# Optimization experiments

Measured on AMD Instinct MI355X. Metric: run time of the kernel, lower is better.

Reference implementation:

```python
import jax, jax.numpy as jnp
import numpy as np

NEG_SLOPE = 0.01  # nn.LeakyReLU default


def leaky_relu(x):
    return jnp.where(x >= 0, x, NEG_SLOPE * x)


def gcn_conv(x, W, b, src, dst, n_nodes):
    """PyG GCNConv: add self loops, symmetric D^-1/2 (A+I) D^-1/2 norm, then x @ W + b."""
    h = x @ W  # [N, D]
    # degree with self-loops (edge weight 1 each, +1 for the self loop)
    deg = jnp.zeros((n_nodes,), dtype=x.dtype).at[dst].add(1.0) + 1.0
    dinv = jax.lax.rsqrt(deg)  # deg >= 1 thanks to self loops
    norm = dinv[src] * dinv[dst]  # [E]
    msg = h[src] * norm[:, None]  # gather + scale, [E, D]
    agg = jnp.zeros_like(h).at[dst].add(msg)  # scatter-add over targets
    agg = agg + h * (dinv * dinv)[:, None]  # self-loop contribution
    return agg + b


def setup_inputs() -> dict:
    key = jax.random.key(0)
    ks = jax.random.split(key, 12)
    N, E = 100000, 640000
    ND, D, C = 239, 128, 2
    x = jax.random.normal(ks[0], (N, ND), dtype=jnp.float32)
    edge_index = jax.random.randint(ks[1], (2, E), 0, N, dtype=jnp.int64)
    edge_type = jax.random.randint(ks[2], (E,), 0, 4, dtype=jnp.int64)
    s = 0.05
    W_in = jax.random.normal(ks[3], (ND, D), dtype=jnp.float32) * s
    b_in = jax.random.normal(ks[4], (D,), dtype=jnp.float32) * s
    W_g = jax.random.normal(ks[5], (D, D), dtype=jnp.float32) * s
    b_g = jax.random.normal(ks[6], (D,), dtype=jnp.float32) * s
    W_o1 = jax.random.normal(ks[7], (D, D), dtype=jnp.float32) * s
    b_o1 = jax.random.normal(ks[8], (D,), dtype=jnp.float32) * s
    W_o2 = jax.random.normal(ks[9], (D, C), dtype=jnp.float32) * s
    b_o2 = jax.random.normal(ks[10], (C,), dtype=jnp.float32) * s
    return {"x": x, "edge_index": edge_index, "edge_type": edge_type,
            "W_in": W_in, "b_in": b_in, "W_g": W_g, "b_g": b_g,
            "W_o1": W_o1, "b_o1": b_o1, "W_o2": W_o2, "b_o2": b_o2}


def reference(x, edge_index, edge_type, W_in, b_in, W_g, b_g, W_o1, b_o1, W_o2, b_o2):
    n_nodes = x.shape[0]
    src, dst = edge_index[0], edge_index[1]
    h = leaky_relu(x @ W_in + b_in)
    h = gcn_conv(h, W_g, b_g, src, dst, n_nodes)
    # dropout is identity in eval mode (training=False)
    h = gcn_conv(h, W_g, b_g, src, dst, n_nodes)  # same shared GCNConv instance
    h = leaky_relu(h @ W_o1 + b_o1)
    return h @ W_o2 + b_o2
```

## Files before the change

kernel.cpp:

```cpp
#include <hip/hip_runtime.h>
#include <hip/hip_bf16.h>


typedef __attribute__((ext_vector_type(8))) __bf16 bf16x8;
typedef __attribute__((ext_vector_type(4))) float f32x4;

__global__ __launch_bounds__(256) void wtr_k(const float* __restrict__ W, ushort* __restrict__ Wt,
                                             int K, int Kp) {
  int idx = blockIdx.x * 256 + threadIdx.x;
  if (idx >= 128 * Kp) return;
  int n = idx / Kp, k = idx % Kp;
  float v = (k < K) ? W[(size_t)k * 128 + n] : 0.f;
  __hip_bfloat16 h = __float2bfloat16(v);
  Wt[idx] = *(ushort*)&h;
}


__global__ __launch_bounds__(256) void zero_k(int* __restrict__ p, int n) {
  int i = blockIdx.x * 256 + threadIdx.x;
  if (i < n) p[i] = 0;
}

__global__ __launch_bounds__(256) void hist_k(const int* __restrict__ dst, int* __restrict__ cnt, int E) {
  int e = blockIdx.x * 256 + threadIdx.x;
  if (e < E) atomicAdd(&cnt[dst[e]], 1);
}

__global__ __launch_bounds__(256) void scan1_k(const int* __restrict__ cnt, int* __restrict__ rp,
                                               int* __restrict__ bsum, int N) {
  __shared__ int sd[256];
  int t = threadIdx.x;
  int base = blockIdx.x * 1024 + t * 4;
  int v0 = (base + 0 < N) ? cnt[base + 0] : 0;
  int v1 = (base + 1 < N) ? cnt[base + 1] : 0;
  int v2 = (base + 2 < N) ? cnt[base + 2] : 0;
  int v3 = (base + 3 < N) ? cnt[base + 3] : 0;
  int ts = v0 + v1 + v2 + v3;
  sd[t] = ts;
  __syncthreads();
  for (int off = 1; off < 256; off <<= 1) {
    int y = (t >= off) ? sd[t - off] : 0;
    __syncthreads();
    sd[t] += y;
    __syncthreads();
  }
  int x = sd[t] - ts;
  if (t == 255) bsum[blockIdx.x] = sd[255];
  if (base + 0 < N) rp[base + 0] = x; x += v0;
  if (base + 1 < N) rp[base + 1] = x; x += v1;
  if (base + 2 < N) rp[base + 2] = x; x += v2;
  if (base + 3 < N) rp[base + 3] = x;
}

__global__ __launch_bounds__(256) void scan2_k(int* __restrict__ bsum, int NB) {
  __shared__ int sd[256];
  int t = threadIdx.x;
  int base = t * 4;
  int v0 = (base + 0 < NB) ? bsum[base + 0] : 0;
  int v1 = (base + 1 < NB) ? bsum[base + 1] : 0;
  int v2 = (base + 2 < NB) ? bsum[base + 2] : 0;
  int v3 = (base + 3 < NB) ? bsum[base + 3] : 0;
  int ts = v0 + v1 + v2 + v3;
  sd[t] = ts;
  __syncthreads();
  for (int off = 1; off < 256; off <<= 1) {
    int y = (t >= off) ? sd[t - off] : 0;
    __syncthreads();
    sd[t] += y;
    __syncthreads();
  }
  int x = sd[t] - ts;
  if (base + 0 < NB) bsum[base + 0] = x; x += v0;
  if (base + 1 < NB) bsum[base + 1] = x; x += v1;
  if (base + 2 < NB) bsum[base + 2] = x; x += v2;
  if (base + 3 < NB) bsum[base + 3] = x;
}

__global__ __launch_bounds__(256) void scan3_k(int* __restrict__ rp, int* __restrict__ pos,
                                               const int* __restrict__ bsum,
                                               float* __restrict__ dinv, int N, int E) {
  int i = blockIdx.x * 256 + threadIdx.x;
  if (i < N) {
    int c = pos[i];
    int v = rp[i] + bsum[i >> 10];
    dinv[i] = rsqrtf((float)c + 1.0f);
    rp[i] = v;
    pos[i] = v;
  }
  if (i == 0) rp[N] = E;
}

__global__ __launch_bounds__(256) void fill_k(const int* __restrict__ src, const int* __restrict__ dst,
                                              const float* __restrict__ dinv,
                                              int* __restrict__ pos, int2* __restrict__ ew, int E) {
  int e = blockIdx.x * 256 + threadIdx.x;
  if (e < E) {
    int d = dst[e];
    int s = src[e];
    int idx = atomicAdd(&pos[d], 1);
    ew[idx] = make_int2(s, __float_as_int(dinv[s] * dinv[d]));
  }
}


__global__ __launch_bounds__(512, 4) void gemm1_k(const float* __restrict__ x,
                                                  const ushort* __restrict__ Wt,
                                                  const float* __restrict__ bias,
                                                  ushort* __restrict__ C, int N, int Ka,
                                                  unsigned long long M ) {
  __shared__ ushort Al[128 * 248];
  __shared__ ushort Wl[128 * 72];
  const int tid = threadIdx.x;
  const int wave = tid >> 6;
  const int lane = tid & 63;
  const int l16 = lane & 15;
  const int quad = lane >> 4;
  const int m0 = blockIdx.x * 128;

  if (tid < 128) {
    Al[tid * 248 + 239] = 0;
    *(uint4*)&Al[tid * 248 + 240] = make_uint4(0, 0, 0, 0);
  }

  {
    int rows = N - m0;
    if (rows > 128) rows = 128;
    const int region = rows * Ka;
    const float* __restrict__ xb = x + (size_t)m0 * Ka;
    const int nv4 = region >> 2;
    for (int i = tid; i < nv4; i += 512) {
      float4 v = ((const float4*)xb)[i];
      int f0 = i * 4;
      float vf[4] = {v.x, v.y, v.z, v.w};
#pragma unroll
      for (int j = 0; j < 4; ++j) {
        int idx = f0 + j;
        uint r = (uint)(((unsigned long long)(uint)idx * M) >> 40);
        uint c = (uint)idx - r * (uint)Ka;
        __hip_bfloat16 h = __float2bfloat16(vf[j]);
        Al[r * 248 + c] = *(ushort*)&h;
      }
    }
    for (int i = (nv4 << 2) + tid; i < region; i += 512) {
      uint r = (uint)(((unsigned long long)(uint)i * M) >> 40);
      uint c = (uint)i - r * (uint)Ka;
      __hip_bfloat16 h = __float2bfloat16(xb[i]);
      Al[r * 248 + c] = *(ushort*)&h;
    }
  }

  f32x4 acc[8] = {};
  const int wn = tid >> 2;
  const int wseg = tid & 3;
#pragma unroll
  for (int kc = 0; kc < 4; ++kc) {
    __syncthreads();
    *(uint4*)&Wl[wn * 72 + wseg * 16] =
        *(const uint4*)(Wt + (size_t)wn * 256 + kc * 64 + wseg * 16);
    *(uint4*)&Wl[wn * 72 + wseg * 16 + 8] =
        *(const uint4*)(Wt + (size_t)wn * 256 + kc * 64 + wseg * 16 + 8);
    __syncthreads();
#pragma unroll
    for (int s = 0; s < 2; ++s) {
      const int koff = kc * 64 + s * 32 + quad * 8;
      bf16x8 a = {};
      if (koff < 248) a = *(const bf16x8*)&Al[(wave * 16 + l16) * 248 + koff];
      const int wof = s * 32 + quad * 8;
#pragma unroll
      for (int c = 0; c < 8; ++c) {
        bf16x8 b = *(const bf16x8*)&Wl[(c * 16 + l16) * 72 + wof];
        acc[c] = __builtin_amdgcn_mfma_f32_16x16x32_bf16(a, b, acc[c], 0, 0, 0);
      }
    }
  }

  float bv[8];
#pragma unroll
  for (int c = 0; c < 8; ++c) bv[c] = bias[c * 16 + l16];
#pragma unroll
  for (int reg = 0; reg < 4; ++reg) {
    int row = m0 + wave * 16 + quad * 4 + reg;
    if (row < N) {
#pragma unroll
      for (int c = 0; c < 8; ++c) {
        float v = acc[c][reg] + bv[c];
        v = v >= 0.f ? v : 0.01f * v;
        __hip_bfloat16 h = __float2bfloat16(v);
        C[(size_t)row * 128 + c * 16 + l16] = *(ushort*)&h;
      }
    }
  }
}


template <int MODE>
__global__ __launch_bounds__(512, 4) void mgemm_k(const ushort* __restrict__ A,
                                                  const ushort* __restrict__ Wt,
                                                  const float* __restrict__ bias,
                                                  const float* __restrict__ W2,
                                                  const float* __restrict__ b2,
                                                  void* __restrict__ C, int N) {
  __shared__ uint4 Al[128 * 16];
  __shared__ uint4 Wl[128 * 16];
  const int tid = threadIdx.x;
  const int wave = tid >> 6;
  const int lane = tid & 63;
  const int l16 = lane & 15;
  const int quad = lane >> 4;
  const int m0 = blockIdx.x * 128;

  f32x4 acc[8] = {};
  const int r_s = tid >> 4;
  const int j8 = tid & 15;
#pragma unroll
  for (int it = 0; it < 4; ++it) {
    int m = it * 32 + r_s;
    Al[m * 16 + (j8 ^ (m & 15))] = *(const uint4*)(A + (size_t)(m0 + m) * 128 + j8 * 8);
  }
#pragma unroll
  for (int it = 0; it < 4; ++it) {
    int n = it * 32 + r_s;
    Wl[n * 16 + (j8 ^ (n & 15))] = *(const uint4*)(Wt + (size_t)n * 128 + j8 * 8);
  }
  __syncthreads();
#pragma unroll
  for (int s = 0; s < 4; ++s) {
    const int j = s * 4 + quad;
    const int arow = wave * 16 + l16;
    bf16x8 a = *(const bf16x8*)&Al[arow * 16 + (j ^ (arow & 15))];
#pragma unroll
    for (int c = 0; c < 8; ++c) {
      const int brow = c * 16 + l16;
      bf16x8 b = *(const bf16x8*)&Wl[brow * 16 + (j ^ (brow & 15))];
      acc[c] = __builtin_amdgcn_mfma_f32_16x16x32_bf16(a, b, acc[c], 0, 0, 0);
    }
  }

  float bv[8];
#pragma unroll
  for (int c = 0; c < 8; ++c) bv[c] = bias[c * 16 + l16];

  if constexpr (MODE == 3) {
    float w20[8], w21[8];
#pragma unroll
    for (int c = 0; c < 8; ++c) {
      int colj = c * 16 + l16;
      w20[c] = W2[colj * 2 + 0];
      w21[c] = W2[colj * 2 + 1];
    }
    float bb0 = b2[0], bb1 = b2[1];
#pragma unroll
    for (int reg = 0; reg < 4; ++reg) {
      float o0 = 0.f, o1 = 0.f;
#pragma unroll
      for (int c = 0; c < 8; ++c) {
        float v = acc[c][reg] + bv[c];
        v = v >= 0.f ? v : 0.01f * v;
        o0 = fmaf(v, w20[c], o0);
        o1 = fmaf(v, w21[c], o1);
      }
      o0 += __shfl_xor(o0, 1); o0 += __shfl_xor(o0, 2);
      o0 += __shfl_xor(o0, 4); o0 += __shfl_xor(o0, 8);
      o1 += __shfl_xor(o1, 1); o1 += __shfl_xor(o1, 2);
      o1 += __shfl_xor(o1, 4); o1 += __shfl_xor(o1, 8);
      int row = m0 + wave * 16 + quad * 4 + reg;
      if (l16 == 0 && row < N)
        *(float2*)((float*)C + (size_t)row * 2) = make_float2(o0 + bb0, o1 + bb1);
    }
    return;
  }

#pragma unroll
  for (int reg = 0; reg < 4; ++reg) {
    int row = m0 + wave * 16 + quad * 4 + reg;
    if (row < N) {
#pragma unroll
      for (int c = 0; c < 8; ++c) {
        float v = acc[c][reg] + bv[c];
        __hip_bfloat16 h = __float2bfloat16(v);
        ((ushort*)C)[(size_t)row * 128 + c * 16 + l16] = *(ushort*)&h;
      }
    }
  }
}


__global__ __launch_bounds__(256) void agg_k(const ushort* __restrict__ T,
                                             const float* __restrict__ dinv,
                                             const int* __restrict__ rp,
                                             const int2* __restrict__ ew,
                                             ushort* __restrict__ O, int N) {
  int l = threadIdx.x & 15;
  int node = blockIdx.x * 16 + (threadIdx.x >> 4);
  if (node >= N) return;
  float di = dinv[node];
  float dsq = di * di;
  const uint4* T4 = (const uint4*)T;
  float a[8];
  {
    uint4 sv = T4[(size_t)node * 16 + l];
    uint u[4] = {sv.x, sv.y, sv.z, sv.w};
#pragma unroll
    for (int p = 0; p < 4; ++p) {
      a[2 * p + 0] = __uint_as_float(u[p] << 16) * dsq;
      a[2 * p + 1] = __uint_as_float(u[p] & 0xFFFF0000u) * dsq;
    }
  }
  int e1 = rp[node + 1];
  for (int e = rp[node]; e < e1; ++e) {
    int2 pw = ew[e];
    float w = __int_as_float(pw.y);
    uint4 v = T4[(size_t)pw.x * 16 + l];
    uint u[4] = {v.x, v.y, v.z, v.w};
#pragma unroll
    for (int p = 0; p < 4; ++p) {
      a[2 * p + 0] = fmaf(__uint_as_float(u[p] << 16), w, a[2 * p + 0]);
      a[2 * p + 1] = fmaf(__uint_as_float(u[p] & 0xFFFF0000u), w, a[2 * p + 1]);
    }
  }
  union { uint4 v; ushort s[8]; } uo;
#pragma unroll
  for (int j = 0; j < 8; ++j) {
    __hip_bfloat16 h = __float2bfloat16(a[j]);
    uo.s[j] = *(ushort*)&h;
  }
  ((uint4*)O)[(size_t)node * 16 + l] = uo.v;
}


extern "C" void kernel_launch(void* const* d_in, const int* in_sizes, int n_in,
                              void* d_out, int out_size, void* d_ws, size_t ws_size,
                              hipStream_t stream) {
  const float* x = (const float*)d_in[0];
  const int* ei = (const int*)d_in[1];
  const float* W_in = (const float*)d_in[3];
  const float* b_in = (const float*)d_in[4];
  const float* W_g  = (const float*)d_in[5];
  const float* b_g  = (const float*)d_in[6];
  const float* W_o1 = (const float*)d_in[7];
  const float* b_o1 = (const float*)d_in[8];
  const float* W_o2 = (const float*)d_in[9];
  const float* b_o2 = (const float*)d_in[10];

  const int D = in_sizes[4];
  const int ND = in_sizes[3] / D;
  const int N = in_sizes[0] / ND;
  const int E = in_sizes[2];
  const int* src = ei;
  const int* dst = ei + E;

  const int N_pad = ((N + 127) / 128) * 128;
  const size_t np = (size_t)N_pad;
  const int KP1 = 256;
  const unsigned long long MAGIC = ((1ULL << 40) + (unsigned)ND - 1) / (unsigned)ND;

  ushort* hA = (ushort*)d_ws;
  ushort* hB = hA + np * 128;
  ushort* Wt_in = hB + np * 128;
  ushort* Wt_g  = Wt_in + 128 * 256;
  ushort* Wt_o1 = Wt_g + 128 * 128;
  float* dinv = (float*)(Wt_o1 + 128 * 128);
  int* cnt  = (int*)(dinv + N);
  int* rp   = cnt + N;
  int* bsum = rp + (N + 1);
  int2* ew  = (int2*)(((size_t)(bsum + 1024) + 7) & ~(size_t)7);

  const int NB = (N + 1023) / 1024;

  wtr_k<<<(128 * KP1 + 255) / 256, 256, 0, stream>>>(W_in, Wt_in, ND, KP1);
  wtr_k<<<(128 * 128 + 255) / 256, 256, 0, stream>>>(W_g, Wt_g, 128, 128);
  wtr_k<<<(128 * 128 + 255) / 256, 256, 0, stream>>>(W_o1, Wt_o1, 128, 128);

  zero_k<<<(N + 255) / 256, 256, 0, stream>>>(cnt, N);
  hist_k<<<(E + 255) / 256, 256, 0, stream>>>(dst, cnt, E);
  scan1_k<<<NB, 256, 0, stream>>>(cnt, rp, bsum, N);
  scan2_k<<<1, 256, 0, stream>>>(bsum, NB);
  scan3_k<<<(N + 255) / 256, 256, 0, stream>>>(rp, cnt , bsum, dinv, N, E);
  fill_k<<<(E + 255) / 256, 256, 0, stream>>>(src, dst, dinv, cnt, ew, E);

  const int gblocks = N_pad / 128;
  const int ablocks = (N + 15) / 16;
  gemm1_k<<<gblocks, 512, 0, stream>>>(x, Wt_in, b_in, hA, N, ND, MAGIC);
  agg_k<<<ablocks, 256, 0, stream>>>(hA, dinv, rp, ew, hB, N);
  mgemm_k<1><<<gblocks, 512, 0, stream>>>(hB, Wt_g, b_g, nullptr, nullptr, hA, N);
  agg_k<<<ablocks, 256, 0, stream>>>(hA, dinv, rp, ew, hB, N);
  mgemm_k<1><<<gblocks, 512, 0, stream>>>(hB, Wt_g, b_g, nullptr, nullptr, hA, N);
  mgemm_k<3><<<gblocks, 512, 0, stream>>>(hA, Wt_o1, b_o1, W_o2, b_o2, d_out, N);
}
```

Baseline: 365.8 us.

## Split aggregation edges across four sub-groups per node and batch x loads in gemm1

agg_k now assigns one 64-lane wave per node, with four 16-lane groups each handling every fourth incoming edge. The partial sums are combined with xor shuffles, which gives more memory-level parallelism on the gathered rows. In gemm1 the x staging loop issues eight float4 loads before converting any of them, and it replaces the per-element division-by-magic with a single row computation plus a boundary bump. The cost is that agg_k launches four times as many threads, which sit idle when a node has few edges, plus the extra shuffle work.

```diff
diff --git a/kernel.cpp b/kernel.cpp
--- a/kernel.cpp
+++ b/kernel.cpp
@@ -128,17 +128,30 @@
     const int region = rows * Ka;
     const float* __restrict__ xb = x + (size_t)m0 * Ka;
     const int nv4 = region >> 2;
-    for (int i = tid; i < nv4; i += 512) {
-      float4 v = ((const float4*)xb)[i];
-      int f0 = i * 4;
-      float vf[4] = {v.x, v.y, v.z, v.w};
-#pragma unroll
-      for (int j = 0; j < 4; ++j) {
-        int idx = f0 + j;
-        uint r = (uint)(((unsigned long long)(uint)idx * M) >> 40);
-        uint c = (uint)idx - r * (uint)Ka;
-        __hip_bfloat16 h = __float2bfloat16(vf[j]);
-        Al[r * 248 + c] = *(ushort*)&h;
+    const uint bump = 248u - (uint)Ka;
+    for (int i0 = tid; i0 < nv4; i0 += 512 * 8) {
+      float4 v[8];
+#pragma unroll
+      for (int b = 0; b < 8; ++b) {
+        int i = i0 + b * 512;
+        if (i < nv4) v[b] = ((const float4*)xb)[i];
+      }
+#pragma unroll
+      for (int b = 0; b < 8; ++b) {
+        int i = i0 + b * 512;
+        if (i < nv4) {
+          uint idx = (uint)i * 4u;
+          uint r = (uint)(((unsigned long long)idx * M) >> 40);
+          uint c = idx - r * (uint)Ka;
+          uint a0 = r * 248u + c;
+          float vf[4] = {v[b].x, v[b].y, v[b].z, v[b].w};
+#pragma unroll
+          for (int j = 0; j < 4; ++j) {
+            uint adr = a0 + j + ((c + j >= (uint)Ka) ? bump : 0u);
+            __hip_bfloat16 h = __float2bfloat16(vf[j]);
+            Al[adr] = *(ushort*)&h;
+          }
+        }
       }
     }
     for (int i = (nv4 << 2) + tid; i < region; i += 512) {
@@ -290,14 +303,17 @@
                                              const int* __restrict__ rp,
                                              const int2* __restrict__ ew,
                                              ushort* __restrict__ O, int N) {
-  int l = threadIdx.x & 15;
-  int node = blockIdx.x * 16 + (threadIdx.x >> 4);
+  const int node = blockIdx.x * 4 + (threadIdx.x >> 6);
   if (node >= N) return;
-  float di = dinv[node];
-  float dsq = di * di;
+  const int lane = threadIdx.x & 63;
+  const int es = lane >> 4;
+  const int l = lane & 15;
   const uint4* T4 = (const uint4*)T;
-  float a[8];
-  {
+
+  float a[8] = {0.f, 0.f, 0.f, 0.f, 0.f, 0.f, 0.f, 0.f};
+  if (es == 0) {
+    float di = dinv[node];
+    float dsq = di * di;
     uint4 sv = T4[(size_t)node * 16 + l];
     uint u[4] = {sv.x, sv.y, sv.z, sv.w};
 #pragma unroll
@@ -306,10 +322,13 @@
       a[2 * p + 1] = __uint_as_float(u[p] & 0xFFFF0000u) * dsq;
     }
   }
-  int e1 = rp[node + 1];
-  for (int e = rp[node]; e < e1; ++e) {
-    int2 pw = ew[e];
-    float w = __int_as_float(pw.y);
+
+  const int e0 = rp[node], e1 = rp[node + 1];
+  for (int eb = e0; eb < e1; eb += 4) {
+    int e = eb + es;
+    bool act = e < e1;
+    int2 pw = ew[act ? e : e0];
+    float w = act ? __int_as_float(pw.y) : 0.f;
     uint4 v = T4[(size_t)pw.x * 16 + l];
     uint u[4] = {v.x, v.y, v.z, v.w};
 #pragma unroll
@@ -318,13 +337,22 @@
       a[2 * p + 1] = fmaf(__uint_as_float(u[p] & 0xFFFF0000u), w, a[2 * p + 1]);
     }
   }
-  union { uint4 v; ushort s[8]; } uo;
+
 #pragma unroll
   for (int j = 0; j < 8; ++j) {
-    __hip_bfloat16 h = __float2bfloat16(a[j]);
-    uo.s[j] = *(ushort*)&h;
-  }
-  ((uint4*)O)[(size_t)node * 16 + l] = uo.v;
+    a[j] += __shfl_xor(a[j], 16);
+    a[j] += __shfl_xor(a[j], 32);
+  }
+
+  if (es == 0) {
+    union { uint4 v; ushort s[8]; } uo;
+#pragma unroll
+    for (int j = 0; j < 8; ++j) {
+      __hip_bfloat16 h = __float2bfloat16(a[j]);
+      uo.s[j] = *(ushort*)&h;
+    }
+    ((uint4*)O)[(size_t)node * 16 + l] = uo.v;
+  }
 }
 
 
@@ -379,7 +407,7 @@
   fill_k<<<(E + 255) / 256, 256, 0, stream>>>(src, dst, dinv, cnt, ew, E);
 
   const int gblocks = N_pad / 128;
-  const int ablocks = (N + 15) / 16;
+  const int ablocks = (N + 3) / 4;
   gemm1_k<<<gblocks, 512, 0, stream>>>(x, Wt_in, b_in, hA, N, ND, MAGIC);
   agg_k<<<ablocks, 256, 0, stream>>>(hA, dinv, rp, ew, hB, N);
   mgemm_k<1><<<gblocks, 512, 0, stream>>>(hB, Wt_g, b_g, nullptr, nullptr, hA, N);
```

New measurement: 376.2 us. 1.03x slower.
